# Kernel tuning notes

Hardware: AMD Instinct MI355X
Metric: run time of the kernel (lower is better)

## Reference

```python
import jax, jax.numpy as jnp
import numpy as np

EPS = 1e-6  # torch.nn.PairwiseDistance default eps, added to the difference before norm
B, D, H, W = 2048, 1024, 128, 128


def setup_inputs() -> dict:
    key = jax.random.key(0)
    k1, k2 = jax.random.split(key)
    x = jax.random.normal(k1, (B, D), dtype=jnp.float32)
    # SOM codebook: [input_size, H*W], matches torch.randn(input_size, out_size[0]*out_size[1])
    weight = jax.random.normal(k2, (D, H * W), dtype=jnp.float32)
    # grid locations, row-major (x, y) as produced by get_map_index()
    gx, gy = jnp.meshgrid(jnp.arange(H), jnp.arange(W), indexing='ij')
    locations = jnp.stack([gx.ravel(), gy.ravel()], axis=1).astype(jnp.float32)  # [H*W, 2]
    return {"x": x, "weight": weight, "locations": locations}


def reference(x, weight, locations):
    # dists[b, m] = || x[b] - weight[:, m] + EPS ||_2  (PairwiseDistance p=2 semantics)
    d = x.shape[1]
    sq = (jnp.sum(x * x, axis=1, keepdims=True)          # [B, 1]
          + jnp.sum(weight * weight, axis=0)[None, :]    # [1, M]
          - 2.0 * (x @ weight)                            # [B, M] GEMM
          + 2.0 * EPS * (jnp.sum(x, axis=1, keepdims=True) - jnp.sum(weight, axis=0)[None, :])
          + d * EPS * EPS)
    dists = jnp.sqrt(jnp.maximum(sq, 0.0))                # [B, M]
    losses = jnp.min(dists, axis=1, keepdims=True)        # [B, 1]
    bmu_indexes = jnp.argmin(dists, axis=1, keepdims=True)  # [B, 1] int
    bmu_locations = locations[bmu_indexes]                 # [B, 1, 2]
    loss = jnp.sum(losses) / x.shape[0]                    # scalar mean min-distance
    return bmu_indexes, bmu_locations, loss
```

## Files before the change

kernel.cpp:

```cpp
#include <hip/hip_runtime.h>
#include <cstdint>
#include <cstddef>


#define B_  2048
#define D_  1024
#define M_  16384
#define EPS_ 1e-6f

typedef _Float16 v8h __attribute__((ext_vector_type(8)));
typedef _Float16 v4h __attribute__((ext_vector_type(4)));
typedef float    v4f __attribute__((ext_vector_type(4)));

static __device__ __forceinline__ unsigned long long umin64(unsigned long long a,
                                                            unsigned long long b) {
    return a < b ? a : b;
}

#define GLDS16(g, l)                                                            \
    __builtin_amdgcn_global_load_lds(                                           \
        (const __attribute__((address_space(1))) void*)(g),                     \
        (__attribute__((address_space(3))) void*)(l), 16, 0, 0)

__global__ void xconv(const float* __restrict__ x,
                      _Float16* __restrict__ xh, _Float16* __restrict__ xl,
                      float* __restrict__ rowTerm) {
    int b = blockIdx.x;
    int t = threadIdx.x;
    const float4 v = *(const float4*)(x + (size_t)b * D_ + t * 4);
    v4h h, l;
    float acc = 0.f;
    float vv[4] = {v.x, v.y, v.z, v.w};
    #pragma unroll
    for (int e = 0; e < 4; ++e) {
        _Float16 hi = (_Float16)vv[e];
        float lo = vv[e] - (float)hi;
        h[e] = hi; l[e] = (_Float16)lo;
        acc += vv[e] * vv[e] + 2.0f * EPS_ * vv[e];
    }
    *(v4h*)(xh + (size_t)b * D_ + t * 4) = h;
    *(v4h*)(xl + (size_t)b * D_ + t * 4) = l;
    for (int off = 32; off; off >>= 1) acc += __shfl_down(acc, off, 64);
    __shared__ float s[4];
    if ((t & 63) == 0) s[t >> 6] = acc;
    __syncthreads();
    if (t == 0) rowTerm[b] = s[0] + s[1] + s[2] + s[3];
}

__global__ void wconv(const float* __restrict__ W,
                      _Float16* __restrict__ wth, _Float16* __restrict__ wtl,
                      float* __restrict__ colTerm) {
    __shared__ float tile[64][65];
    const int t = threadIdx.x;
    const int m0 = blockIdx.x * 64;
    const int d0 = blockIdx.y * 64;
    const int dloc = t >> 4, mq = (t & 15) * 4;
    #pragma unroll
    for (int s = 0; s < 4; ++s) {
        float4 v = *(const float4*)(W + (size_t)(d0 + dloc + 16 * s) * M_ + m0 + mq);
        tile[dloc + 16 * s][mq + 0] = v.x;
        tile[dloc + 16 * s][mq + 1] = v.y;
        tile[dloc + 16 * s][mq + 2] = v.z;
        tile[dloc + 16 * s][mq + 3] = v.w;
    }
    __syncthreads();
    const int dc = (t & 7) * 8;
    #pragma unroll
    for (int p = 0; p < 2; ++p) {
        int mloc = (t >> 3) + 32 * p;
        v8h h, l;
        float acc = 0.f;
        #pragma unroll
        for (int e = 0; e < 8; ++e) {
            float v = tile[dc + e][mloc];
            _Float16 hi = (_Float16)v;
            float lo = v - (float)hi;
            h[e] = hi; l[e] = (_Float16)lo;
            acc += v * v - 2.0f * EPS_ * v;
        }
        *(v8h*)(wth + (size_t)(m0 + mloc) * D_ + d0 + dc) = h;
        *(v8h*)(wtl + (size_t)(m0 + mloc) * D_ + d0 + dc) = l;
        acc += __shfl_down(acc, 4, 8);
        acc += __shfl_down(acc, 2, 8);
        acc += __shfl_down(acc, 1, 8);
        if ((t & 7) == 0) atomicAdd(&colTerm[m0 + mloc], acc);
    }
}

__global__ __launch_bounds__(256, 2) void som_mfma(
    const _Float16* __restrict__ xh, const _Float16* __restrict__ xl,
    const _Float16* __restrict__ wth, const _Float16* __restrict__ wtl,
    const float* __restrict__ rowTerm, const float* __restrict__ colTerm,
    unsigned long long* __restrict__ keys)
{
    __shared__ __align__(16) _Float16 smem[16384];
    _Float16* Ah = smem;
    _Float16* Al = smem + 4096;
    _Float16* Bh = smem + 8192;
    _Float16* Bl = smem + 12288;

    const int t  = threadIdx.x;
    const int rb = blockIdx.y * 128;
    const int cb = blockIdx.x * 128;
    const int L  = t & 63, w = t >> 6;
    const int wro = (w >> 1) * 64, wco = (w & 1) * 64;
    const int c16 = L & 15, kq = L >> 4;

    const int u1 = t, u2 = t + 256;
    const size_t aoff1 = (size_t)(rb + (u1 >> 2)) * 2048 + (u1 & 3) * 16;
    const size_t aoff2 = (size_t)(rb + (u2 >> 2)) * 2048 + (u2 & 3) * 16;
    const size_t boff1 = (size_t)(cb + (u1 >> 2)) * 2048 + (u1 & 3) * 16;
    const size_t boff2 = (size_t)(cb + (u2 >> 2)) * 2048 + (u2 & 3) * 16;
    const int lds1 = (t & 192) * 16;
    const int lds2 = (256 + (t & 192)) * 16;
    const char* pxh = (const char*)xh;
    const char* pxl = (const char*)xl;
    const char* pwh = (const char*)wth;
    const char* pwl = (const char*)wtl;

    v4f acc[4][4];
    #pragma unroll
    for (int i = 0; i < 4; ++i)
        #pragma unroll
        for (int j = 0; j < 4; ++j) acc[i][j] = (v4f){0.f, 0.f, 0.f, 0.f};

    for (int kb = 0; kb < 2048; kb += 64) {
        __syncthreads();
        GLDS16(pxh + aoff1 + kb, (char*)Ah + lds1);
        GLDS16(pxh + aoff2 + kb, (char*)Ah + lds2);
        GLDS16(pxl + aoff1 + kb, (char*)Al + lds1);
        GLDS16(pxl + aoff2 + kb, (char*)Al + lds2);
        GLDS16(pwh + boff1 + kb, (char*)Bh + lds1);
        GLDS16(pwh + boff2 + kb, (char*)Bh + lds2);
        GLDS16(pwl + boff1 + kb, (char*)Bl + lds1);
        GLDS16(pwl + boff2 + kb, (char*)Bl + lds2);
        __syncthreads();

        v8h ah[4], al4[4], bh[4], bl4[4];
        #pragma unroll
        for (int i = 0; i < 4; ++i) {
            int ra = (wro + i * 16 + c16) * 32 + kq * 8;
            int rbx = (wco + i * 16 + c16) * 32 + kq * 8;
            ah[i]  = *(const v8h*)(Ah + ra);
            al4[i] = *(const v8h*)(Al + ra);
            bh[i]  = *(const v8h*)(Bh + rbx);
            bl4[i] = *(const v8h*)(Bl + rbx);
        }
        #pragma unroll
        for (int i = 0; i < 4; ++i)
            #pragma unroll
            for (int j = 0; j < 4; ++j) {
                acc[i][j] = __builtin_amdgcn_mfma_f32_16x16x32_f16(ah[i],  bh[j],  acc[i][j], 0, 0, 0);
                acc[i][j] = __builtin_amdgcn_mfma_f32_16x16x32_f16(ah[i],  bl4[j], acc[i][j], 0, 0, 0);
                acc[i][j] = __builtin_amdgcn_mfma_f32_16x16x32_f16(al4[i], bh[j],  acc[i][j], 0, 0, 0);
            }
    }

    float cT[4];
    #pragma unroll
    for (int j = 0; j < 4; ++j) cT[j] = colTerm[cb + wco + j * 16 + c16];
    const float de2 = (float)D_ * EPS_ * EPS_;
    #pragma unroll
    for (int i = 0; i < 4; ++i) {
        #pragma unroll
        for (int r = 0; r < 4; ++r) {
            int row_g = rb + wro + i * 16 + kq * 4 + r;
            float rt = rowTerm[row_g];
            unsigned long long best = ~0ull;
            #pragma unroll
            for (int j = 0; j < 4; ++j) {
                float sq = rt + cT[j] - 2.0f * acc[i][j][r] + de2;
                sq = fmaxf(sq, 0.0f);
                float dist = sqrtf(sq);
                unsigned long long key =
                    ((unsigned long long)__float_as_uint(dist) << 32) |
                    (unsigned int)(cb + wco + j * 16 + c16);
                best = umin64(best, key);
            }
            #pragma unroll
            for (int m = 1; m <= 8; m <<= 1) {
                unsigned long long o =
                    (unsigned long long)__shfl_xor((long long)best, m, 64);
                best = umin64(best, o);
            }
            if (c16 == 0) atomicMin(&keys[row_g], best);
        }
    }
}

__global__ void row_stats(const float* __restrict__ x, float* __restrict__ rowTerm) {
    int b = blockIdx.x;
    const float* xr = x + (size_t)b * D_;
    int t = threadIdx.x;
    float acc = 0.f;
    for (int i = t; i < D_; i += 256) {
        float v = xr[i];
        acc += v * v + 2.0f * EPS_ * v;
    }
    for (int off = 32; off; off >>= 1) acc += __shfl_down(acc, off, 64);
    __shared__ float s[4];
    if ((t & 63) == 0) s[t >> 6] = acc;
    __syncthreads();
    if (t == 0) rowTerm[b] = s[0] + s[1] + s[2] + s[3];
}

__global__ void col_stats(const float* __restrict__ w, float* __restrict__ colTerm) {
    int m = blockIdx.x * 256 + threadIdx.x;
    int d0 = blockIdx.y * 64;
    const float* p = w + (size_t)d0 * M_ + m;
    float acc = 0.f;
    #pragma unroll 8
    for (int d = 0; d < 64; ++d) {
        float v = p[(size_t)d * M_];
        acc += v * v - 2.0f * EPS_ * v;
    }
    atomicAdd(&colTerm[m], acc);
}

__global__ __launch_bounds__(256, 2) void som_gemm(
    const float* __restrict__ A, const float* __restrict__ Wt,
    const float* __restrict__ rowTerm, const float* __restrict__ colTerm,
    unsigned long long* __restrict__ keys)
{
    __shared__ float As[8][128];
    __shared__ float Bs[8][128];
    const int t  = threadIdx.x;
    const int rb = blockIdx.y * 128;
    const int cb = blockIdx.x * 128;
    const int tx = t & 15;
    const int ty = t >> 4;
    float acc[8][8];
    #pragma unroll
    for (int i = 0; i < 8; ++i)
        #pragma unroll
        for (int j = 0; j < 8; ++j) acc[i][j] = 0.f;
    const int la_row = t >> 1, la_k = (t & 1) * 4;
    const int lb_k = t >> 5, lb_n = (t & 31) * 4;
    const float* Aptr = A + (size_t)(rb + la_row) * D_ + la_k;
    const float* Bptr = Wt + (size_t)lb_k * M_ + cb + lb_n;
    for (int k0 = 0; k0 < D_; k0 += 8) {
        float4 av = *(const float4*)(Aptr + k0);
        float4 bv = *(const float4*)(Bptr + (size_t)k0 * M_);
        __syncthreads();
        As[la_k + 0][la_row] = av.x;
        As[la_k + 1][la_row] = av.y;
        As[la_k + 2][la_row] = av.z;
        As[la_k + 3][la_row] = av.w;
        *(float4*)&Bs[lb_k][lb_n] = bv;
        __syncthreads();
        #pragma unroll
        for (int k = 0; k < 8; ++k) {
            float a[8], b[8];
            #pragma unroll
            for (int i = 0; i < 8; ++i) a[i] = As[k][ty * 8 + i];
            #pragma unroll
            for (int j = 0; j < 8; ++j) b[j] = Bs[k][tx * 8 + j];
            #pragma unroll
            for (int i = 0; i < 8; ++i)
                #pragma unroll
                for (int j = 0; j < 8; ++j) acc[i][j] += a[i] * b[j];
        }
    }
    float rT[8], cT[8];
    #pragma unroll
    for (int i = 0; i < 8; ++i) rT[i] = rowTerm[rb + ty * 8 + i];
    #pragma unroll
    for (int j = 0; j < 8; ++j) cT[j] = colTerm[cb + tx * 8 + j];
    const float de2 = (float)D_ * EPS_ * EPS_;
    #pragma unroll
    for (int i = 0; i < 8; ++i) {
        unsigned long long best = ~0ull;
        #pragma unroll
        for (int j = 0; j < 8; ++j) {
            float sq = rT[i] + cT[j] - 2.0f * acc[i][j] + de2;
            sq = fmaxf(sq, 0.0f);
            float dist = sqrtf(sq);
            unsigned long long key =
                ((unsigned long long)__float_as_uint(dist) << 32) |
                (unsigned int)(cb + tx * 8 + j);
            best = umin64(best, key);
        }
        #pragma unroll
        for (int msk = 1; msk <= 8; msk <<= 1) {
            unsigned long long o = __shfl_xor((long long)best, msk, 64);
            best = umin64(best, (unsigned long long)o);
        }
        if (tx == 0) atomicMin(&keys[rb + ty * 8 + i], best);
    }
}

__global__ void finalize(const unsigned long long* __restrict__ keys,
                         const float* __restrict__ loc,
                         float* __restrict__ out)
{
    int t = threadIdx.x;
    float sum = 0.f;
    for (int r = t; r < B_; r += 256) {
        unsigned long long k = keys[r];
        unsigned int idx = (unsigned int)(k & 0xFFFFFFFFu);
        float dist = __uint_as_float((unsigned int)(k >> 32));
        out[r] = (float)idx;
        out[B_ + 2 * r]     = loc[2 * idx];
        out[B_ + 2 * r + 1] = loc[2 * idx + 1];
        sum += dist;
    }
    for (int off = 32; off; off >>= 1) sum += __shfl_down(sum, off, 64);
    __shared__ float s[4];
    if ((t & 63) == 0) s[t >> 6] = sum;
    __syncthreads();
    if (t == 0) out[3 * B_] = (s[0] + s[1] + s[2] + s[3]) / (float)B_;
}

extern "C" void kernel_launch(void* const* d_in, const int* in_sizes, int n_in,
                              void* d_out, int out_size, void* d_ws, size_t ws_size,
                              hipStream_t stream)
{
    const float* x   = (const float*)d_in[0];
    const float* w   = (const float*)d_in[1];
    const float* loc = (const float*)d_in[2];
    float* out = (float*)d_out;

    char* ws = (char*)d_ws;
    unsigned long long* keys = (unsigned long long*)ws;
    float* rowTerm = (float*)(ws + (16 << 10));
    float* colTerm = (float*)(ws + (24 << 10));
    _Float16* xh  = (_Float16*)(ws + (1ull << 20));
    _Float16* xl  = (_Float16*)(ws + (5ull << 20));
    _Float16* wth = (_Float16*)(ws + (9ull << 20));
    _Float16* wtl = (_Float16*)(ws + (41ull << 20));
    const size_t NEED = 73ull << 20;

    hipMemsetAsync(keys, 0xFF, B_ * sizeof(unsigned long long), stream);
    hipMemsetAsync(colTerm, 0, M_ * sizeof(float), stream);

    if (ws_size >= NEED) {
        xconv<<<B_, 256, 0, stream>>>(x, xh, xl, rowTerm);
        wconv<<<dim3(M_ / 64, D_ / 64), 256, 0, stream>>>(w, wth, wtl, colTerm);
        som_mfma<<<dim3(M_ / 128, B_ / 128), 256, 0, stream>>>(
            xh, xl, wth, wtl, rowTerm, colTerm, keys);
    } else {
        row_stats<<<B_, 256, 0, stream>>>(x, rowTerm);
        col_stats<<<dim3(M_ / 256, D_ / 64), 256, 0, stream>>>(w, colTerm);
        som_gemm<<<dim3(M_ / 128, B_ / 128), 256, 0, stream>>>(
            x, w, rowTerm, colTerm, keys);
    }
    finalize<<<1, 256, 0, stream>>>(keys, loc, out);
}
```

Before: 356.3 us.

## Switch SOM GEMM to 32x32x16 MFMA with XOR-swizzled LDS layout and parallel finalize

Replaces the 16x16x32 MFMA tiling in the split-fp16 distance GEMM with 32x32x16 MFMA tiles. Each wave now loads fewer fragments per k-step, which cuts LDS reads per MFMA. The global-to-LDS chunk placement is XOR-swizzled to reduce LDS bank conflicts on fragment reads, and the argmin epilogue is reworked for the 32-lane layout. The finalize kernel now runs across 8 blocks and accumulates the loss with an atomicAdd into a pre-zeroed output, which adds a memset and makes the float sum order nondeterministic.

```diff
diff --git a/kernel.cpp b/kernel.cpp
--- a/kernel.cpp
+++ b/kernel.cpp
@@ -8,9 +8,10 @@
 #define M_  16384
 #define EPS_ 1e-6f
 
-typedef _Float16 v8h __attribute__((ext_vector_type(8)));
-typedef _Float16 v4h __attribute__((ext_vector_type(4)));
-typedef float    v4f __attribute__((ext_vector_type(4)));
+typedef _Float16 v8h  __attribute__((ext_vector_type(8)));
+typedef _Float16 v4h  __attribute__((ext_vector_type(4)));
+typedef float    v4f  __attribute__((ext_vector_type(4)));
+typedef float    v16f __attribute__((ext_vector_type(16)));
 
 static __device__ __forceinline__ unsigned long long umin64(unsigned long long a,
                                                             unsigned long long b) {
@@ -104,25 +105,41 @@
     const int cb = blockIdx.x * 128;
     const int L  = t & 63, w = t >> 6;
     const int wro = (w >> 1) * 64, wco = (w & 1) * 64;
-    const int c16 = L & 15, kq = L >> 4;
-
-    const int u1 = t, u2 = t + 256;
-    const size_t aoff1 = (size_t)(rb + (u1 >> 2)) * 2048 + (u1 & 3) * 16;
-    const size_t aoff2 = (size_t)(rb + (u2 >> 2)) * 2048 + (u2 & 3) * 16;
-    const size_t boff1 = (size_t)(cb + (u1 >> 2)) * 2048 + (u1 & 3) * 16;
-    const size_t boff2 = (size_t)(cb + (u2 >> 2)) * 2048 + (u2 & 3) * 16;
+    const int l31 = L & 31, q = L >> 5;
+
+    const int m1 = t >> 2;
+    const int c1 = (t & 3) ^ (m1 & 3);
+    const size_t aoff1 = (size_t)(rb + m1) * 2048 + c1 * 16;
+    const size_t aoff2 = aoff1 + 64ull * 2048;
+    const size_t boff1 = (size_t)(cb + m1) * 2048 + c1 * 16;
+    const size_t boff2 = boff1 + 64ull * 2048;
     const int lds1 = (t & 192) * 16;
-    const int lds2 = (256 + (t & 192)) * 16;
+    const int lds2 = lds1 + 4096;
     const char* pxh = (const char*)xh;
     const char* pxl = (const char*)xl;
     const char* pwh = (const char*)wth;
     const char* pwl = (const char*)wtl;
 
-    v4f acc[4][4];
-    #pragma unroll
-    for (int i = 0; i < 4; ++i)
-        #pragma unroll
-        for (int j = 0; j < 4; ++j) acc[i][j] = (v4f){0.f, 0.f, 0.f, 0.f};
+    v16f acc[2][2];
+    #pragma unroll
+    for (int i = 0; i < 2; ++i)
+        #pragma unroll
+        for (int j = 0; j < 2; ++j)
+            #pragma unroll
+            for (int r = 0; r < 16; ++r) acc[i][j][r] = 0.f;
+
+    int ia[2][2], ib[2][2];
+    #pragma unroll
+    for (int ti = 0; ti < 2; ++ti) {
+        int mA = wro + ti * 32 + l31;
+        int mB = wco + ti * 32 + l31;
+        #pragma unroll
+        for (int h = 0; h < 2; ++h) {
+            int ch = h * 2 + q;
+            ia[ti][h] = (mA * 4 + (ch ^ (mA & 3))) * 8;
+            ib[ti][h] = (mB * 4 + (ch ^ (mB & 3))) * 8;
+        }
+    }
 
     for (int kb = 0; kb < 2048; kb += 64) {
         __syncthreads();
@@ -136,54 +153,59 @@
         GLDS16(pwl + boff2 + kb, (char*)Bl + lds2);
         __syncthreads();
 
-        v8h ah[4], al4[4], bh[4], bl4[4];
-        #pragma unroll
-        for (int i = 0; i < 4; ++i) {
-            int ra = (wro + i * 16 + c16) * 32 + kq * 8;
-            int rbx = (wco + i * 16 + c16) * 32 + kq * 8;
-            ah[i]  = *(const v8h*)(Ah + ra);
-            al4[i] = *(const v8h*)(Al + ra);
-            bh[i]  = *(const v8h*)(Bh + rbx);
-            bl4[i] = *(const v8h*)(Bl + rbx);
-        }
-        #pragma unroll
-        for (int i = 0; i < 4; ++i)
-            #pragma unroll
-            for (int j = 0; j < 4; ++j) {
-                acc[i][j] = __builtin_amdgcn_mfma_f32_16x16x32_f16(ah[i],  bh[j],  acc[i][j], 0, 0, 0);
-                acc[i][j] = __builtin_amdgcn_mfma_f32_16x16x32_f16(ah[i],  bl4[j], acc[i][j], 0, 0, 0);
-                acc[i][j] = __builtin_amdgcn_mfma_f32_16x16x32_f16(al4[i], bh[j],  acc[i][j], 0, 0, 0);
+        v8h fah[2][2], fal[2][2], fbh[2][2], fbl[2][2];
+        #pragma unroll
+        for (int ti = 0; ti < 2; ++ti)
+            #pragma unroll
+            for (int h = 0; h < 2; ++h) {
+                fah[ti][h] = *(const v8h*)(Ah + ia[ti][h]);
+                fal[ti][h] = *(const v8h*)(Al + ia[ti][h]);
+                fbh[ti][h] = *(const v8h*)(Bh + ib[ti][h]);
+                fbl[ti][h] = *(const v8h*)(Bl + ib[ti][h]);
             }
-    }
-
-    float cT[4];
-    #pragma unroll
-    for (int j = 0; j < 4; ++j) cT[j] = colTerm[cb + wco + j * 16 + c16];
+        #pragma unroll
+        for (int ti = 0; ti < 2; ++ti)
+            #pragma unroll
+            for (int tj = 0; tj < 2; ++tj)
+                #pragma unroll
+                for (int h = 0; h < 2; ++h) {
+                    acc[ti][tj] = __builtin_amdgcn_mfma_f32_32x32x16_f16(
+                        fah[ti][h], fbh[tj][h], acc[ti][tj], 0, 0, 0);
+                    acc[ti][tj] = __builtin_amdgcn_mfma_f32_32x32x16_f16(
+                        fah[ti][h], fbl[tj][h], acc[ti][tj], 0, 0, 0);
+                    acc[ti][tj] = __builtin_amdgcn_mfma_f32_32x32x16_f16(
+                        fal[ti][h], fbh[tj][h], acc[ti][tj], 0, 0, 0);
+                }
+    }
+
+    float cT[2];
+    #pragma unroll
+    for (int tj = 0; tj < 2; ++tj) cT[tj] = colTerm[cb + wco + tj * 32 + l31];
     const float de2 = (float)D_ * EPS_ * EPS_;
     #pragma unroll
-    for (int i = 0; i < 4; ++i) {
-        #pragma unroll
-        for (int r = 0; r < 4; ++r) {
-            int row_g = rb + wro + i * 16 + kq * 4 + r;
+    for (int ti = 0; ti < 2; ++ti) {
+        #pragma unroll
+        for (int reg = 0; reg < 16; ++reg) {
+            int row_g = rb + wro + ti * 32 + (reg & 3) + 8 * (reg >> 2) + 4 * q;
             float rt = rowTerm[row_g];
             unsigned long long best = ~0ull;
             #pragma unroll
-            for (int j = 0; j < 4; ++j) {
-                float sq = rt + cT[j] - 2.0f * acc[i][j][r] + de2;
+            for (int tj = 0; tj < 2; ++tj) {
+                float sq = rt + cT[tj] - 2.0f * acc[ti][tj][reg] + de2;
                 sq = fmaxf(sq, 0.0f);
                 float dist = sqrtf(sq);
                 unsigned long long key =
                     ((unsigned long long)__float_as_uint(dist) << 32) |
-                    (unsigned int)(cb + wco + j * 16 + c16);
+                    (unsigned int)(cb + wco + tj * 32 + l31);
                 best = umin64(best, key);
             }
             #pragma unroll
-            for (int m = 1; m <= 8; m <<= 1) {
+            for (int m = 1; m <= 16; m <<= 1) {
                 unsigned long long o =
                     (unsigned long long)__shfl_xor((long long)best, m, 64);
                 best = umin64(best, o);
             }
-            if (c16 == 0) atomicMin(&keys[row_g], best);
+            if (l31 == 0) atomicMin(&keys[row_g], best);
         }
     }
 }
@@ -294,21 +316,19 @@
                          float* __restrict__ out)
 {
     int t = threadIdx.x;
-    float sum = 0.f;
-    for (int r = t; r < B_; r += 256) {
-        unsigned long long k = keys[r];
-        unsigned int idx = (unsigned int)(k & 0xFFFFFFFFu);
-        float dist = __uint_as_float((unsigned int)(k >> 32));
-        out[r] = (float)idx;
-        out[B_ + 2 * r]     = loc[2 * idx];
-        out[B_ + 2 * r + 1] = loc[2 * idx + 1];
-        sum += dist;
-    }
+    int r = blockIdx.x * 256 + t;
+    unsigned long long k = keys[r];
+    unsigned int idx = (unsigned int)(k & 0xFFFFFFFFu);
+    float dist = __uint_as_float((unsigned int)(k >> 32));
+    out[r] = (float)idx;
+    out[B_ + 2 * r]     = loc[2 * idx];
+    out[B_ + 2 * r + 1] = loc[2 * idx + 1];
+    float sum = dist;
     for (int off = 32; off; off >>= 1) sum += __shfl_down(sum, off, 64);
     __shared__ float s[4];
     if ((t & 63) == 0) s[t >> 6] = sum;
     __syncthreads();
-    if (t == 0) out[3 * B_] = (s[0] + s[1] + s[2] + s[3]) / (float)B_;
+    if (t == 0) atomicAdd(&out[3 * B_], (s[0] + s[1] + s[2] + s[3]) / (float)B_);
 }
 
 extern "C" void kernel_launch(void* const* d_in, const int* in_sizes, int n_in,
@@ -332,6 +352,7 @@
 
     hipMemsetAsync(keys, 0xFF, B_ * sizeof(unsigned long long), stream);
     hipMemsetAsync(colTerm, 0, M_ * sizeof(float), stream);
+    hipMemsetAsync(out + 3 * B_, 0, sizeof(float), stream);
 
     if (ws_size >= NEED) {
         xconv<<<B_, 256, 0, stream>>>(x, xh, xl, rowTerm);
@@ -344,5 +365,5 @@
         som_gemm<<<dim3(M_ / 128, B_ / 128), 256, 0, stream>>>(
             x, w, rowTerm, colTerm, keys);
     }
-    finalize<<<1, 256, 0, stream>>>(keys, loc, out);
-}
+    finalize<<<8, 256, 0, stream>>>(keys, loc, out);
+}
```

New measurement: 384.7 us. 1.08x slower.

## Swizzle GEMM LDS tiles into MFMA fragment order and parallelize finalize

Applied to the files above, without the earlier changes.

Changes the global-to-LDS load mapping so each wave stores 16 rows by 64 bytes contiguously in MFMA fragment order, letting each lane read its fragment with a simple contiguous offset and avoiding LDS bank conflicts. The weight conversion kernel now has each thread emit 16 contiguous halves with one reduction step less. Finalize is spread over 8 blocks, with the mean loss accumulated atomically after a memset. The atomic float sum makes the loss order-dependent in rounding.

```diff
diff --git a/kernel.cpp b/kernel.cpp
--- a/kernel.cpp
+++ b/kernel.cpp
@@ -64,27 +64,31 @@
         tile[dloc + 16 * s][mq + 3] = v.w;
     }
     __syncthreads();
-    const int dc = (t & 7) * 8;
-    #pragma unroll
-    for (int p = 0; p < 2; ++p) {
-        int mloc = (t >> 3) + 32 * p;
-        v8h h, l;
-        float acc = 0.f;
-        #pragma unroll
-        for (int e = 0; e < 8; ++e) {
-            float v = tile[dc + e][mloc];
-            _Float16 hi = (_Float16)v;
-            float lo = v - (float)hi;
-            h[e] = hi; l[e] = (_Float16)lo;
-            acc += v * v - 2.0f * EPS_ * v;
-        }
-        *(v8h*)(wth + (size_t)(m0 + mloc) * D_ + d0 + dc) = h;
-        *(v8h*)(wtl + (size_t)(m0 + mloc) * D_ + d0 + dc) = l;
-        acc += __shfl_down(acc, 4, 8);
-        acc += __shfl_down(acc, 2, 8);
-        acc += __shfl_down(acc, 1, 8);
-        if ((t & 7) == 0) atomicAdd(&colTerm[m0 + mloc], acc);
-    }
+    const int mloc = t >> 2;
+    const int dc = (t & 3) * 16;
+    v8h h0, l0, h1, l1;
+    float acc = 0.f;
+    #pragma unroll
+    for (int e = 0; e < 8; ++e) {
+        float v = tile[dc + e][mloc];
+        _Float16 hi = (_Float16)v;
+        h0[e] = hi; l0[e] = (_Float16)(v - (float)hi);
+        acc += v * v - 2.0f * EPS_ * v;
+    }
+    #pragma unroll
+    for (int e = 0; e < 8; ++e) {
+        float v = tile[dc + 8 + e][mloc];
+        _Float16 hi = (_Float16)v;
+        h1[e] = hi; l1[e] = (_Float16)(v - (float)hi);
+        acc += v * v - 2.0f * EPS_ * v;
+    }
+    _Float16* oh = wth + (size_t)(m0 + mloc) * D_ + d0 + dc;
+    _Float16* ol = wtl + (size_t)(m0 + mloc) * D_ + d0 + dc;
+    *(v8h*)oh = h0; *(v8h*)(oh + 8) = h1;
+    *(v8h*)ol = l0; *(v8h*)(ol + 8) = l1;
+    acc += __shfl_xor(acc, 1, 64);
+    acc += __shfl_xor(acc, 2, 64);
+    if ((t & 3) == 0) atomicAdd(&colTerm[m0 + mloc], acc);
 }
 
 __global__ __launch_bounds__(256, 2) void som_mfma(
@@ -106,13 +110,14 @@
     const int wro = (w >> 1) * 64, wco = (w & 1) * 64;
     const int c16 = L & 15, kq = L >> 4;
 
-    const int u1 = t, u2 = t + 256;
-    const size_t aoff1 = (size_t)(rb + (u1 >> 2)) * 2048 + (u1 & 3) * 16;
-    const size_t aoff2 = (size_t)(rb + (u2 >> 2)) * 2048 + (u2 & 3) * 16;
-    const size_t boff1 = (size_t)(cb + (u1 >> 2)) * 2048 + (u1 & 3) * 16;
-    const size_t boff2 = (size_t)(cb + (u2 >> 2)) * 2048 + (u2 & 3) * 16;
+    const int row0 = ((t >> 6) << 4) + (t & 15);
+    const int ch0  = (t >> 4) & 3;
+    const size_t aoff1 = (size_t)(rb + row0) * 2048 + ch0 * 16;
+    const size_t aoff2 = aoff1 + 64ull * 2048;
+    const size_t boff1 = (size_t)(cb + row0) * 2048 + ch0 * 16;
+    const size_t boff2 = boff1 + 64ull * 2048;
     const int lds1 = (t & 192) * 16;
-    const int lds2 = (256 + (t & 192)) * 16;
+    const int lds2 = lds1 + 4096;
     const char* pxh = (const char*)xh;
     const char* pxl = (const char*)xl;
     const char* pwh = (const char*)wth;
@@ -123,6 +128,13 @@
     for (int i = 0; i < 4; ++i)
         #pragma unroll
         for (int j = 0; j < 4; ++j) acc[i][j] = (v4f){0.f, 0.f, 0.f, 0.f};
+
+    int ia[4], ib[4];
+    #pragma unroll
+    for (int i = 0; i < 4; ++i) {
+        ia[i] = ((wro >> 4) + i) * 512 + L * 8;
+        ib[i] = ((wco >> 4) + i) * 512 + L * 8;
+    }
 
     for (int kb = 0; kb < 2048; kb += 64) {
         __syncthreads();
@@ -139,12 +151,10 @@
         v8h ah[4], al4[4], bh[4], bl4[4];
         #pragma unroll
         for (int i = 0; i < 4; ++i) {
-            int ra = (wro + i * 16 + c16) * 32 + kq * 8;
-            int rbx = (wco + i * 16 + c16) * 32 + kq * 8;
-            ah[i]  = *(const v8h*)(Ah + ra);
-            al4[i] = *(const v8h*)(Al + ra);
-            bh[i]  = *(const v8h*)(Bh + rbx);
-            bl4[i] = *(const v8h*)(Bl + rbx);
+            ah[i]  = *(const v8h*)(Ah + ia[i]);
+            al4[i] = *(const v8h*)(Al + ia[i]);
+            bh[i]  = *(const v8h*)(Bh + ib[i]);
+            bl4[i] = *(const v8h*)(Bl + ib[i]);
         }
         #pragma unroll
         for (int i = 0; i < 4; ++i)
@@ -294,21 +304,19 @@
                          float* __restrict__ out)
 {
     int t = threadIdx.x;
-    float sum = 0.f;
-    for (int r = t; r < B_; r += 256) {
-        unsigned long long k = keys[r];
-        unsigned int idx = (unsigned int)(k & 0xFFFFFFFFu);
-        float dist = __uint_as_float((unsigned int)(k >> 32));
-        out[r] = (float)idx;
-        out[B_ + 2 * r]     = loc[2 * idx];
-        out[B_ + 2 * r + 1] = loc[2 * idx + 1];
-        sum += dist;
-    }
+    int r = blockIdx.x * 256 + t;
+    unsigned long long k = keys[r];
+    unsigned int idx = (unsigned int)(k & 0xFFFFFFFFu);
+    float dist = __uint_as_float((unsigned int)(k >> 32));
+    out[r] = (float)idx;
+    out[B_ + 2 * r]     = loc[2 * idx];
+    out[B_ + 2 * r + 1] = loc[2 * idx + 1];
+    float sum = dist;
     for (int off = 32; off; off >>= 1) sum += __shfl_down(sum, off, 64);
     __shared__ float s[4];
     if ((t & 63) == 0) s[t >> 6] = sum;
     __syncthreads();
-    if (t == 0) out[3 * B_] = (s[0] + s[1] + s[2] + s[3]) / (float)B_;
+    if (t == 0) atomicAdd(&out[3 * B_], (s[0] + s[1] + s[2] + s[3]) / (float)B_);
 }
 
 extern "C" void kernel_launch(void* const* d_in, const int* in_sizes, int n_in,
@@ -332,6 +340,7 @@
 
     hipMemsetAsync(keys, 0xFF, B_ * sizeof(unsigned long long), stream);
     hipMemsetAsync(colTerm, 0, M_ * sizeof(float), stream);
+    hipMemsetAsync(out + 3 * B_, 0, sizeof(float), stream);
 
     if (ws_size >= NEED) {
         xconv<<<B_, 256, 0, stream>>>(x, xh, xl, rowTerm);
@@ -344,5 +353,5 @@
         som_gemm<<<dim3(M_ / 128, B_ / 128), 256, 0, stream>>>(
             x, w, rowTerm, colTerm, keys);
     }
-    finalize<<<1, 256, 0, stream>>>(keys, loc, out);
-}
+    finalize<<<8, 256, 0, stream>>>(keys, loc, out);
+}
```

Result: slower. 402.1 us (+12.8%).
